# Kernel optimization log

Measured on AMD Instinct MI355X. Metric: run time of the kernel, lower is better.

The kernel has to match this reference:

```python
import jax, jax.numpy as jnp
import numpy as np

N_NODES = 50000
N_EDGES = 1_600_000
F_IN = 128
F_OUT = 8
K_TAPS = 4
AVG_DEG = 32.0


def setup_inputs() -> dict:
    key = jax.random.key(0)
    k1, k2, k3, k4, k5 = jax.random.split(key, 5)
    x = jax.random.normal(k1, (N_NODES, F_IN), dtype=jnp.float32)
    gso_rows = jax.random.randint(k2, (N_EDGES,), 0, N_NODES, dtype=jnp.int32)
    gso_cols = jax.random.randint(k3, (N_EDGES,), 0, N_NODES, dtype=jnp.int32)
    gso_vals = jax.random.uniform(k4, (N_EDGES,), dtype=jnp.float32) / AVG_DEG
    # filterCoeff = randn(outFeat, filter_order) * 0.1 as in torch __init__
    coeff = jax.random.normal(k5, (F_OUT, K_TAPS), dtype=jnp.float32) * 0.1
    return {"x": x, "gso_rows": gso_rows, "gso_cols": gso_cols,
            "gso_vals": gso_vals, "coeff": coeff}


def reference(x, gso_rows, gso_cols, gso_vals, coeff):
    # Faithful to the torch code INCLUDING its carried-over SpMV state:
    # output feature o uses powers S^{1+o(K-1)} .. S^{o(K-1)+K} of x.
    F_out, K = coeff.shape
    N = x.shape[0]
    max_power = F_out * (K - 1) + 1  # highest S power needed

    def spmv(Z):  # S @ Z via edge-list gather + segment_sum scatter
        return jax.ops.segment_sum(gso_vals[:, None] * Z[gso_cols], gso_rows,
                                   num_segments=N)

    def step(Z, _):
        Zn = spmv(Z)
        return Zn, Zn.sum(axis=1)  # sum over in-features done up-front

    # s[p-1, n] = sum_f (S^p x)[n, f], for p = 1..max_power
    _, s = jax.lax.scan(step, x, None, length=max_power)  # (max_power, N)

    # power index (0-based into s) used by output o, tap i: o*(K-1) + i
    idx = jnp.arange(F_out)[:, None] * (K - 1) + jnp.arange(K)[None, :]  # (F_out, K)
    sg = s[idx]  # (F_out, K, N)
    y = jnp.einsum('ok,okn->no', coeff, sg)  # (N, F_out)
    return y
```

## Files before the change

kernel.cpp:

```cpp
#include <hip/hip_runtime.h>
#include <hip/hip_bf16.h>

#define N_NODES 50000
#define N_EDGES 1600000
#define F_IN    128
#define F_OUT   8
#define K_TAPS  4
#define MAX_POWER 25

#define BROWS   64
#define NB      782
#define CHUNK   4096
#define NPART   391
#define ECAP    2816

#define BAR_LINES 32
#define LSTRIDE   32

__device__ inline int wave_incl_scan(int v, int lane) {
    #pragma unroll
    for (int off = 1; off < 64; off <<= 1) {
        int t = __shfl_up(v, off, 64);
        if (lane >= off) v += t;
    }
    return v;
}

__device__ inline void st_coh(float* p, float v) {
    __hip_atomic_store(p, v, __ATOMIC_RELAXED, __HIP_MEMORY_SCOPE_AGENT);
}

__global__ void partition_kernel(const int* __restrict__ rows,
                                 const int* __restrict__ cols,
                                 const float* __restrict__ vals,
                                 int* __restrict__ gcnt,
                                 int2* __restrict__ edges, int n_edges) {
    __shared__ int lhist[NB];
    __shared__ int lcur[NB];
    __shared__ int lbase[NB];
    __shared__ int2 stage[CHUNK];
    __shared__ unsigned short sbkt[CHUNK];
    __shared__ int wsum[4];
    int tid = threadIdx.x;
    int base = blockIdx.x * CHUNK;
    int cend = min(base + CHUNK, n_edges);

    for (int b = tid; b < NB; b += 256) lhist[b] = 0;
    __syncthreads();
    for (int i = base + tid; i < cend; i += 256)
        atomicAdd(&lhist[rows[i] >> 6], 1);
    __syncthreads();

    int lane = tid & 63, wid = tid >> 6;
    int b0 = tid * 4;
    int h[4]; int tsum = 0;
    #pragma unroll
    for (int j = 0; j < 4; ++j) {
        h[j] = (b0 + j < NB) ? lhist[b0 + j] : 0;
        tsum += h[j];
    }
    int incl = wave_incl_scan(tsum, lane);
    if (lane == 63) wsum[wid] = incl;
    __syncthreads();
    int woff = 0;
    for (int w = 0; w < wid; ++w) woff += wsum[w];
    int excl = woff + incl - tsum;
    #pragma unroll
    for (int j = 0; j < 4; ++j) {
        if (b0 + j < NB) lcur[b0 + j] = excl;
        excl += h[j];
    }
    __syncthreads();

    for (int b = tid; b < NB; b += 256) {
        int c = lhist[b];
        if (c) {
            int g = atomicAdd(&gcnt[b], c);
            lbase[b] = b * ECAP + g - lcur[b];
        }
    }
    __syncthreads();

    for (int i = base + tid; i < cend; i += 256) {
        int r = rows[i], c = cols[i];
        float v = vals[i];
        int b = r >> 6;
        int pos = atomicAdd(&lcur[b], 1);
        stage[pos] = make_int2(((r & 63) << 16) | c, __float_as_int(v));
        sbkt[pos] = (unsigned short)b;
    }
    __syncthreads();

    int cn = cend - base;
    for (int i = tid; i < cn; i += 256) {
        int b = sbkt[i];
        int o = lbase[b] + i;
        if (o - b * ECAP < ECAP)
            edges[o] = stage[i];
    }
}

__device__ inline void gbar(int it, int b,
                            int* __restrict__ bar_cnt,
                            int* __restrict__ bar_master,
                            int* __restrict__ bar_gen) {
    __syncthreads();
    if (threadIdx.x == 0) {
        int r = b & (BAR_LINES - 1);
        int need = (NB / BAR_LINES) + (r < (NB % BAR_LINES) ? 1 : 0);
        int c = __hip_atomic_fetch_add(&bar_cnt[(it * BAR_LINES + r) * LSTRIDE], 1,
                                       __ATOMIC_RELAXED, __HIP_MEMORY_SCOPE_AGENT);
        if (c == need - 1) {
            int m = __hip_atomic_fetch_add(&bar_master[it * LSTRIDE], 1,
                                           __ATOMIC_RELAXED, __HIP_MEMORY_SCOPE_AGENT);
            if (m == BAR_LINES - 1)
                __hip_atomic_store(bar_gen, it + 1,
                                   __ATOMIC_RELAXED, __HIP_MEMORY_SCOPE_AGENT);
        }
        while (__hip_atomic_load(bar_gen, __ATOMIC_RELAXED,
                                 __HIP_MEMORY_SCOPE_AGENT) < it + 1)
            __builtin_amdgcn_s_sleep(2);
    }
    __syncthreads();
}

__global__ __launch_bounds__(256, 4)
void chain_kernel(const int* __restrict__ gcnt,
                  const int2* __restrict__ edges,
                  const float* __restrict__ x,
                  const float* __restrict__ coeff,
                  float* __restrict__ u,
                  float* __restrict__ s,
                  float* __restrict__ y,
                  int* __restrict__ bar_cnt,
                  int* __restrict__ bar_master,
                  int* __restrict__ bar_gen,
                  int n_nodes) {
    __shared__ int2  ecache[ECAP];
    __shared__ float acc[BROWS];
    __shared__ float yacc[BROWS * F_OUT];
    __shared__ float lcoeff[F_OUT * K_TAPS];

    int tid = threadIdx.x;
    int b = blockIdx.x;

    if (tid < BROWS) acc[tid] = 0.f;
    for (int j = tid; j < BROWS * F_OUT; j += 256) yacc[j] = 0.f;
    if (tid < F_OUT * K_TAPS) lcoeff[tid] = coeff[tid];

    int cnt = min(gcnt[b], ECAP);
    const int2* eb = edges + (size_t)b * ECAP;
    for (int i = tid; i < cnt; i += 256) ecache[i] = eb[i];

    {
        int lane = tid & 63;
        int wave = (b * 256 + tid) >> 6;
        int n_waves = NB * 4;
        for (int node = wave; node < n_nodes; node += n_waves) {
            const float2* xp = (const float2*)(x + (size_t)node * F_IN);
            float2 v = xp[lane];
            float sm = v.x + v.y;
            #pragma unroll
            for (int off = 32; off > 0; off >>= 1)
                sm += __shfl_down(sm, off, 64);
            if (lane == 0) st_coh(&u[node], sm);
        }
    }
    gbar(0, b, bar_cnt, bar_master, bar_gen);

    for (int p = 0; p < MAX_POWER; ++p) {
        const float* __restrict__ src = (p == 0) ? u : s + (size_t)(p - 1) * n_nodes;
        float* dst = s + (size_t)p * n_nodes;

        for (int i = tid; i < cnt; i += 256) {
            int2 ev = ecache[i];
            float sv = src[ev.x & 0xFFFF];
            atomicAdd(&acc[ev.x >> 16], __int_as_float(ev.y) * sv);
        }
        __syncthreads();

        if (tid < BROWS) {
            int row = b * BROWS + tid;
            float val = acc[tid];
            acc[tid] = 0.f;
            if (p < MAX_POWER - 1 && row < n_nodes) st_coh(&dst[row], val);
            #pragma unroll
            for (int o = 0; o < F_OUT; ++o) {
                int k = p - (K_TAPS - 1) * o;
                if (k >= 0 && k < K_TAPS)
                    yacc[tid * F_OUT + o] += lcoeff[o * K_TAPS + k] * val;
            }
        }
        if (p < MAX_POWER - 1)
            gbar(p + 1, b, bar_cnt, bar_master, bar_gen);
    }

    __syncthreads();
    for (int j = tid; j < BROWS * F_OUT; j += 256) {
        int row = b * BROWS + (j >> 3);
        if (row < n_nodes) y[(size_t)row * F_OUT + (j & 7)] = yacc[j];
    }
}

extern "C" void kernel_launch(void* const* d_in, const int* in_sizes, int n_in,
                              void* d_out, int out_size, void* d_ws, size_t ws_size,
                              hipStream_t stream) {
    const float* x        = (const float*)d_in[0];
    const int*   gso_rows = (const int*)d_in[1];
    const int*   gso_cols = (const int*)d_in[2];
    const float* gso_vals = (const float*)d_in[3];
    const float* coeff    = (const float*)d_in[4];
    float* y = (float*)d_out;

    float* u     = (float*)d_ws;
    float* s     = u + N_NODES;
    int2*  edges = (int2*)(s + (size_t)MAX_POWER * N_NODES);
    int*   gcnt       = (int*)(edges + (size_t)NB * ECAP);
    int*   bar_cnt    = gcnt + NB;
    int*   bar_master = bar_cnt + MAX_POWER * BAR_LINES * LSTRIDE;
    int*   bar_gen    = bar_master + MAX_POWER * LSTRIDE;

    size_t ctrl_ints = (size_t)NB + MAX_POWER * BAR_LINES * LSTRIDE
                     + MAX_POWER * LSTRIDE + 1;
    hipMemsetAsync(gcnt, 0, ctrl_ints * sizeof(int), stream);

    partition_kernel<<<NPART, 256, 0, stream>>>(
        gso_rows, gso_cols, gso_vals, gcnt, edges, N_EDGES);

    int n_nodes = N_NODES;
    void* args[] = { (void*)&gcnt, (void*)&edges, (void*)&x, (void*)&coeff,
                     (void*)&u, (void*)&s, (void*)&y,
                     (void*)&bar_cnt, (void*)&bar_master, (void*)&bar_gen,
                     (void*)&n_nodes };
    hipLaunchCooperativeKernel((void*)chain_kernel, dim3(NB), dim3(256),
                               args, 0, stream);
}
```

Measured before the change: 476.4 us.

## Use one 512-thread block per CU with larger row partitions

```diff
diff --git a/kernel.cpp b/kernel.cpp
--- a/kernel.cpp
+++ b/kernel.cpp
@@ -8,13 +8,14 @@
 #define K_TAPS  4
 #define MAX_POWER 25
 
-#define BROWS   64
-#define NB      782
+#define NBLK    256
+#define RPB     196
 #define CHUNK   4096
 #define NPART   391
-#define ECAP    2816
-
-#define BAR_LINES 32
+#define ECAP_G  8192
+#define ECAP_L  6912
+
+#define BAR_LINES 16
 #define LSTRIDE   32
 
 __device__ inline int wave_incl_scan(int v, int lane) {
@@ -35,59 +36,44 @@
                                  const float* __restrict__ vals,
                                  int* __restrict__ gcnt,
                                  int2* __restrict__ edges, int n_edges) {
-    __shared__ int lhist[NB];
-    __shared__ int lcur[NB];
-    __shared__ int lbase[NB];
+    __shared__ int lhist[NBLK];
+    __shared__ int lcur[NBLK];
+    __shared__ int lbase[NBLK];
     __shared__ int2 stage[CHUNK];
-    __shared__ unsigned short sbkt[CHUNK];
+    __shared__ unsigned char sbkt[CHUNK];
     __shared__ int wsum[4];
     int tid = threadIdx.x;
     int base = blockIdx.x * CHUNK;
     int cend = min(base + CHUNK, n_edges);
 
-    for (int b = tid; b < NB; b += 256) lhist[b] = 0;
+    lhist[tid] = 0;
     __syncthreads();
     for (int i = base + tid; i < cend; i += 256)
-        atomicAdd(&lhist[rows[i] >> 6], 1);
+        atomicAdd(&lhist[rows[i] / RPB], 1);
     __syncthreads();
 
     int lane = tid & 63, wid = tid >> 6;
-    int b0 = tid * 4;
-    int h[4]; int tsum = 0;
-    #pragma unroll
-    for (int j = 0; j < 4; ++j) {
-        h[j] = (b0 + j < NB) ? lhist[b0 + j] : 0;
-        tsum += h[j];
-    }
-    int incl = wave_incl_scan(tsum, lane);
+    int h = lhist[tid];
+    int incl = wave_incl_scan(h, lane);
     if (lane == 63) wsum[wid] = incl;
     __syncthreads();
     int woff = 0;
     for (int w = 0; w < wid; ++w) woff += wsum[w];
-    int excl = woff + incl - tsum;
-    #pragma unroll
-    for (int j = 0; j < 4; ++j) {
-        if (b0 + j < NB) lcur[b0 + j] = excl;
-        excl += h[j];
-    }
-    __syncthreads();
-
-    for (int b = tid; b < NB; b += 256) {
-        int c = lhist[b];
-        if (c) {
-            int g = atomicAdd(&gcnt[b], c);
-            lbase[b] = b * ECAP + g - lcur[b];
-        }
+    int excl = woff + incl - h;
+    lcur[tid] = excl;
+    if (h) {
+        int g = atomicAdd(&gcnt[tid], h);
+        lbase[tid] = tid * ECAP_G + g - excl;
     }
     __syncthreads();
 
     for (int i = base + tid; i < cend; i += 256) {
         int r = rows[i], c = cols[i];
         float v = vals[i];
-        int b = r >> 6;
+        int b = r / RPB;
         int pos = atomicAdd(&lcur[b], 1);
-        stage[pos] = make_int2(((r & 63) << 16) | c, __float_as_int(v));
-        sbkt[pos] = (unsigned short)b;
+        stage[pos] = make_int2(((r - b * RPB) << 16) | c, __float_as_int(v));
+        sbkt[pos] = (unsigned char)b;
     }
     __syncthreads();
 
@@ -95,7 +81,7 @@
     for (int i = tid; i < cn; i += 256) {
         int b = sbkt[i];
         int o = lbase[b] + i;
-        if (o - b * ECAP < ECAP)
+        if (o - b * ECAP_G < ECAP_G)
             edges[o] = stage[i];
     }
 }
@@ -107,7 +93,7 @@
     __syncthreads();
     if (threadIdx.x == 0) {
         int r = b & (BAR_LINES - 1);
-        int need = (NB / BAR_LINES) + (r < (NB % BAR_LINES) ? 1 : 0);
+        const int need = NBLK / BAR_LINES;
         int c = __hip_atomic_fetch_add(&bar_cnt[(it * BAR_LINES + r) * LSTRIDE], 1,
                                        __ATOMIC_RELAXED, __HIP_MEMORY_SCOPE_AGENT);
         if (c == need - 1) {
@@ -124,7 +110,7 @@
     __syncthreads();
 }
 
-__global__ __launch_bounds__(256, 4)
+__global__ __launch_bounds__(512, 1)
 void chain_kernel(const int* __restrict__ gcnt,
                   const int2* __restrict__ edges,
                   const float* __restrict__ x,
@@ -136,26 +122,27 @@
                   int* __restrict__ bar_master,
                   int* __restrict__ bar_gen,
                   int n_nodes) {
-    __shared__ int2  ecache[ECAP];
-    __shared__ float acc[BROWS];
-    __shared__ float yacc[BROWS * F_OUT];
+    __shared__ int2  ecache[ECAP_L];
+    __shared__ float acc[RPB];
+    __shared__ float yacc[RPB * F_OUT];
     __shared__ float lcoeff[F_OUT * K_TAPS];
 
     int tid = threadIdx.x;
     int b = blockIdx.x;
 
-    if (tid < BROWS) acc[tid] = 0.f;
-    for (int j = tid; j < BROWS * F_OUT; j += 256) yacc[j] = 0.f;
+    if (tid < RPB) acc[tid] = 0.f;
+    for (int j = tid; j < RPB * F_OUT; j += 512) yacc[j] = 0.f;
     if (tid < F_OUT * K_TAPS) lcoeff[tid] = coeff[tid];
 
-    int cnt = min(gcnt[b], ECAP);
-    const int2* eb = edges + (size_t)b * ECAP;
-    for (int i = tid; i < cnt; i += 256) ecache[i] = eb[i];
+    int cnt = min(gcnt[b], ECAP_G);
+    int cntl = min(cnt, ECAP_L);
+    const int2* eb = edges + (size_t)b * ECAP_G;
+    for (int i = tid; i < cntl; i += 512) ecache[i] = eb[i];
 
     {
         int lane = tid & 63;
-        int wave = (b * 256 + tid) >> 6;
-        int n_waves = NB * 4;
+        int wave = (b * 512 + tid) >> 6;
+        int n_waves = NBLK * 8;
         for (int node = wave; node < n_nodes; node += n_waves) {
             const float2* xp = (const float2*)(x + (size_t)node * F_IN);
             float2 v = xp[lane];
@@ -172,15 +159,33 @@
         const float* __restrict__ src = (p == 0) ? u : s + (size_t)(p - 1) * n_nodes;
         float* dst = s + (size_t)p * n_nodes;
 
-        for (int i = tid; i < cnt; i += 256) {
+        int i = tid;
+        for (; i + 3 * 512 < cntl; i += 4 * 512) {
+            int2 e0 = ecache[i];
+            int2 e1 = ecache[i + 512];
+            int2 e2 = ecache[i + 1024];
+            int2 e3 = ecache[i + 1536];
+            float v0 = src[e0.x & 0xFFFF];
+            float v1 = src[e1.x & 0xFFFF];
+            float v2 = src[e2.x & 0xFFFF];
+            float v3 = src[e3.x & 0xFFFF];
+            atomicAdd(&acc[e0.x >> 16], __int_as_float(e0.y) * v0);
+            atomicAdd(&acc[e1.x >> 16], __int_as_float(e1.y) * v1);
+            atomicAdd(&acc[e2.x >> 16], __int_as_float(e2.y) * v2);
+            atomicAdd(&acc[e3.x >> 16], __int_as_float(e3.y) * v3);
+        }
+        for (; i < cntl; i += 512) {
             int2 ev = ecache[i];
-            float sv = src[ev.x & 0xFFFF];
-            atomicAdd(&acc[ev.x >> 16], __int_as_float(ev.y) * sv);
+            atomicAdd(&acc[ev.x >> 16], __int_as_float(ev.y) * src[ev.x & 0xFFFF]);
+        }
+        for (int k = ECAP_L + tid; k < cnt; k += 512) {
+            int2 ev = eb[k];
+            atomicAdd(&acc[ev.x >> 16], __int_as_float(ev.y) * src[ev.x & 0xFFFF]);
         }
         __syncthreads();
 
-        if (tid < BROWS) {
-            int row = b * BROWS + tid;
+        if (tid < RPB) {
+            int row = b * RPB + tid;
             float val = acc[tid];
             acc[tid] = 0.f;
             if (p < MAX_POWER - 1 && row < n_nodes) st_coh(&dst[row], val);
@@ -196,8 +201,8 @@
     }
 
     __syncthreads();
-    for (int j = tid; j < BROWS * F_OUT; j += 256) {
-        int row = b * BROWS + (j >> 3);
+    for (int j = tid; j < RPB * F_OUT; j += 512) {
+        int row = b * RPB + (j >> 3);
         if (row < n_nodes) y[(size_t)row * F_OUT + (j & 7)] = yacc[j];
     }
 }
@@ -215,12 +220,12 @@
     float* u     = (float*)d_ws;
     float* s     = u + N_NODES;
     int2*  edges = (int2*)(s + (size_t)MAX_POWER * N_NODES);
-    int*   gcnt       = (int*)(edges + (size_t)NB * ECAP);
-    int*   bar_cnt    = gcnt + NB;
+    int*   gcnt       = (int*)(edges + (size_t)NBLK * ECAP_G);
+    int*   bar_cnt    = gcnt + NBLK;
     int*   bar_master = bar_cnt + MAX_POWER * BAR_LINES * LSTRIDE;
     int*   bar_gen    = bar_master + MAX_POWER * LSTRIDE;
 
-    size_t ctrl_ints = (size_t)NB + MAX_POWER * BAR_LINES * LSTRIDE
+    size_t ctrl_ints = (size_t)NBLK + MAX_POWER * BAR_LINES * LSTRIDE
                      + MAX_POWER * LSTRIDE + 1;
     hipMemsetAsync(gcnt, 0, ctrl_ints * sizeof(int), stream);
 
@@ -232,6 +237,6 @@
                      (void*)&u, (void*)&s, (void*)&y,
                      (void*)&bar_cnt, (void*)&bar_master, (void*)&bar_gen,
                      (void*)&n_nodes };
-    hipLaunchCooperativeKernel((void*)chain_kernel, dim3(NB), dim3(256),
+    hipLaunchCooperativeKernel((void*)chain_kernel, dim3(NBLK), dim3(512),
                                args, 0, stream);
 }
```

New measurement: 424.7 us. 10.8% less time.
